# Performance work log

Measured on AMD Instinct MI355X. Metric: run time of the kernel, lower is better.

Reference implementation:

```python
import jax, jax.numpy as jnp
import numpy as np
from jax import lax


def _conv2d(x, w, b, stride):
    # x: [B,C,H,W], w: [O,I,kh,kw], b: [O]
    y = lax.conv_general_dilated(
        x, w, window_strides=(stride, stride), padding='VALID',
        dimension_numbers=('NCHW', 'OIHW', 'NCHW'))
    return y + b[None, :, None, None]


def setup_inputs() -> dict:
    key = jax.random.key(0)
    ks = jax.random.split(key, 4)
    B, C, H, W = 8, 128, 128, 128
    x = jax.random.normal(ks[0], (B, C, H, W), dtype=jnp.float32)
    # conv weights, scaled like torch default init (~1/sqrt(fan_in))
    Wq = jax.random.normal(ks[1], (C, C, 2, 2), dtype=jnp.float32) / np.sqrt(C * 4)
    Wk = jax.random.normal(ks[2], (C, C, 2, 2), dtype=jnp.float32) / np.sqrt(C * 4)
    Wv = jax.random.normal(ks[3], (C, C, 1, 1), dtype=jnp.float32) / np.sqrt(C)
    bq = jnp.zeros((C,), dtype=jnp.float32)
    bk = jnp.zeros((C,), dtype=jnp.float32)
    bv = jnp.zeros((C,), dtype=jnp.float32)
    return {'x': x, 'Wq': Wq, 'bq': bq, 'Wk': Wk, 'bk': bk, 'Wv': Wv, 'bv': bv}


def reference(x, Wq, bq, Wk, bk, Wv, bv):
    B, C, H, W = x.shape
    # query/key: 2x2 stride-2 convs -> [B, C, (H//2)*(W//2)]
    q = _conv2d(x, Wq, bq, 2).reshape(B, C, -1)
    k = _conv2d(x, Wk, bk, 2).reshape(B, C, -1)
    # value: 1x1 conv -> [B, C, H*W]
    v = _conv2d(x, Wv, bv, 1).reshape(B, C, -1)
    # energy: [B, C, C]
    energy = jnp.einsum('bcn,bdn->bcd', q, k)
    # max-subtract trick: softmax over (row_max - energy)
    energy_new = jnp.max(energy, axis=-1, keepdims=True) - energy
    attention = jax.nn.softmax(energy_new, axis=-1)
    out = jnp.einsum('bcd,bdn->bcn', attention, v)
    return out.reshape(B, C, H, W)
```

## Files before the change

### kernel.cpp

```cpp
#include <hip/hip_runtime.h>
#include <math.h>


typedef float f32x4 __attribute__((ext_vector_type(4)));
typedef short s16x8 __attribute__((ext_vector_type(8)));

__device__ __forceinline__ unsigned short f2bf(float f) {
  union { __bf16 b; unsigned short u; } v;
  v.b = (__bf16)f;
  return v.u;
}
__device__ __forceinline__ float bf2f(unsigned short h) {
  union { unsigned u; float f; } v; v.u = ((unsigned)h) << 16;
  return v.f;
}
__device__ __forceinline__ unsigned pack2(unsigned short a, unsigned short b) {
  return (unsigned)a | ((unsigned)b << 16);
}

__global__ __launch_bounds__(256) void k_prep(
    const float* __restrict__ Wq, const float* __restrict__ Wk,
    unsigned short* __restrict__ Wth, unsigned short* __restrict__ Wtl) {
  const int f = (blockIdx.x * 256 + threadIdx.x) * 4;
  const int row = f >> 9;
  const int k   = f & 511;
  const float* src = (row < 128) ? &Wq[row * 512 + k] : &Wk[(row - 128) * 512 + k];
  float4 v = *(const float4*)src;
  unsigned short h0 = f2bf(v.x), h1 = f2bf(v.y), h2 = f2bf(v.z), h3 = f2bf(v.w);
  unsigned short l0 = f2bf(v.x - bf2f(h0)), l1 = f2bf(v.y - bf2f(h1));
  unsigned short l2 = f2bf(v.z - bf2f(h2)), l3 = f2bf(v.w - bf2f(h3));
  const int di = (k >> 5) * 8192 + row * 32 + (k & 31);
  *(ushort4*)&Wth[di] = make_ushort4(h0, h1, h2, h3);
  *(ushort4*)&Wtl[di] = make_ushort4(l0, l1, l2, l3);
}

__global__ __launch_bounds__(256, 3) void k_conv_energy(
    const float* __restrict__ x,
    const unsigned short* __restrict__ Wth, const unsigned short* __restrict__ Wtl,
    const float* __restrict__ bq, const float* __restrict__ bk,
    float* __restrict__ epart) {
  __shared__ unsigned short LDS[16384];
  unsigned short* Th = LDS;
  unsigned short* Tl = LDS + 8192;

  const int t = threadIdx.x;
  const int nt = blockIdx.x, b = blockIdx.y;
  const int w = t >> 6, lane = t & 63;
  const int lrow = lane & 15, lkb = lane >> 4;

  const int pp = t >> 4;
  const int ci_l = pp >> 1, kh = pp & 1;
  const int i16 = t & 15;
  const int klb = ci_l * 4 + kh * 2;
  const float* xb = x + ((size_t)b << 21);
  const float* xrow = xb + (size_t)ci_l * 16384 + (2 * nt + kh) * 128 + 2 * i16;

  f32x4 acc[4][4];
#pragma unroll
  for (int m = 0; m < 4; ++m)
#pragma unroll
    for (int n = 0; n < 4; ++n) acc[m][n] = (f32x4){0.f, 0.f, 0.f, 0.f};

  s16x8 pfh[4], pfl[4];
  float2 pv[2][4];
  const int aoff = (w * 64 + lrow) * 32 + lkb * 8;

#pragma unroll
  for (int m = 0; m < 4; ++m) {
    pfh[m] = *(const s16x8*)&Wth[aoff + m * 512];
    pfl[m] = *(const s16x8*)&Wtl[aoff + m * 512];
  }
  {
    float2 v0 = *(const float2*)&xrow[0];
    float2 v1 = *(const float2*)&xrow[32];
    float2 v2 = *(const float2*)&xrow[64];
    float2 v3 = *(const float2*)&xrow[96];
    unsigned short hx, hy;
    hx = f2bf(v0.x); hy = f2bf(v0.y);
    *(unsigned*)&LDS[(i16     ) * 40 + klb] = pack2(hx, hy);
    *(unsigned*)&LDS[2560 + (i16     ) * 40 + klb] = pack2(f2bf(v0.x - bf2f(hx)), f2bf(v0.y - bf2f(hy)));
    hx = f2bf(v1.x); hy = f2bf(v1.y);
    *(unsigned*)&LDS[(i16 + 16) * 40 + klb] = pack2(hx, hy);
    *(unsigned*)&LDS[2560 + (i16 + 16) * 40 + klb] = pack2(f2bf(v1.x - bf2f(hx)), f2bf(v1.y - bf2f(hy)));
    hx = f2bf(v2.x); hy = f2bf(v2.y);
    *(unsigned*)&LDS[(i16 + 32) * 40 + klb] = pack2(hx, hy);
    *(unsigned*)&LDS[2560 + (i16 + 32) * 40 + klb] = pack2(f2bf(v2.x - bf2f(hx)), f2bf(v2.y - bf2f(hy)));
    hx = f2bf(v3.x); hy = f2bf(v3.y);
    *(unsigned*)&LDS[(i16 + 48) * 40 + klb] = pack2(hx, hy);
    *(unsigned*)&LDS[2560 + (i16 + 48) * 40 + klb] = pack2(f2bf(v3.x - bf2f(hx)), f2bf(v3.y - bf2f(hy)));
  }
#pragma unroll
  for (int g = 0; g < 4; ++g)
    pv[1][g] = *(const float2*)&xrow[(size_t)8 * 16384 + 32 * g];
  __syncthreads();

#pragma unroll
  for (int step = 0; step < 16; ++step) {
    const int cur = step & 1;
    const unsigned short* Bh = LDS + cur * 5120;
    const unsigned short* Bl = Bh + 2560;
    s16x8 bfh[4], bfl[4];
#pragma unroll
    for (int nf = 0; nf < 4; ++nf) {
      const int bidx = (nf * 16 + lrow) * 40 + lkb * 8;
      bfh[nf] = *(const s16x8*)&Bh[bidx];
      bfl[nf] = *(const s16x8*)&Bl[bidx];
    }
#pragma unroll
    for (int m = 0; m < 4; ++m)
#pragma unroll
      for (int n = 0; n < 4; ++n) {
        acc[m][n] = __builtin_amdgcn_mfma_f32_16x16x32_bf16(pfh[m], bfh[n], acc[m][n], 0, 0, 0);
        acc[m][n] = __builtin_amdgcn_mfma_f32_16x16x32_bf16(pfh[m], bfl[n], acc[m][n], 0, 0, 0);
        acc[m][n] = __builtin_amdgcn_mfma_f32_16x16x32_bf16(pfl[m], bfh[n], acc[m][n], 0, 0, 0);
      }
    if (step < 15) {
      const unsigned short* Wh_n = Wth + (step + 1) * 8192;
      const unsigned short* Wl_n = Wtl + (step + 1) * 8192;
#pragma unroll
      for (int m = 0; m < 4; ++m) {
        pfh[m] = *(const s16x8*)&Wh_n[aoff + m * 512];
        pfl[m] = *(const s16x8*)&Wl_n[aoff + m * 512];
      }
    }
    if (step < 14) {
#pragma unroll
      for (int g = 0; g < 4; ++g)
        pv[cur][g] = *(const float2*)&xrow[(size_t)(step + 2) * 8 * 16384 + 32 * g];
    }
    if (step < 15) {
      unsigned short* Nh = LDS + (cur ^ 1) * 5120;
      unsigned short* Nl = Nh + 2560;
#pragma unroll
      for (int g = 0; g < 4; ++g) {
        const int n = i16 + 16 * g;
        unsigned short hx = f2bf(pv[cur ^ 1][g].x), hy = f2bf(pv[cur ^ 1][g].y);
        *(unsigned*)&Nh[n * 40 + klb] = pack2(hx, hy);
        *(unsigned*)&Nl[n * 40 + klb] = pack2(f2bf(pv[cur ^ 1][g].x - bf2f(hx)),
                                              f2bf(pv[cur ^ 1][g].y - bf2f(hy)));
      }
      asm volatile("s_waitcnt lgkmcnt(0)" ::: "memory");
      __builtin_amdgcn_s_barrier();
    }
  }
  __syncthreads();

  const float* biasp = (w < 2) ? bq : bk;
  const int rb = (w & 1) * 64;
  float biasr[16];
#pragma unroll
  for (int m = 0; m < 4; ++m)
#pragma unroll
    for (int i = 0; i < 4; ++i)
      biasr[m * 4 + i] = biasp[rb + m * 16 + (lane >> 4) * 4 + i];

  f32x4 e[4][4];
#pragma unroll
  for (int m = 0; m < 4; ++m)
#pragma unroll
    for (int n = 0; n < 4; ++n) e[m][n] = (f32x4){0.f, 0.f, 0.f, 0.f};

  const int mrow0 = (w >> 1) * 64;
  const int nrow0 = 128 + (w & 1) * 64;

#pragma unroll
  for (int ks = 0; ks < 2; ++ks) {
#pragma unroll
    for (int m = 0; m < 4; ++m) {
      const int r0 = w * 64 + m * 16 + (lane >> 4) * 4;
#pragma unroll
      for (int nn = 0; nn < 2; ++nn) {
        const int n = 2 * ks + nn;
        const int cl = nn * 16 + lrow;
        const int cl8 = cl >> 3, c7 = cl & 7;
#pragma unroll
        for (int i = 0; i < 4; ++i) {
          const int r = r0 + i;
          const float vv = acc[m][n][i] + biasr[m * 4 + i];
          const unsigned short h = f2bf(vv);
          const unsigned short l = f2bf(vv - bf2f(h));
          const int ad = r * 32 + ((cl8 ^ (r & 3)) << 3) + c7;
          Th[ad] = h;
          Tl[ad] = l;
        }
      }
    }
    __syncthreads();
    {
      s16x8 qh[4], ql[4], kh8[4], kl8[4];
#pragma unroll
      for (int m = 0; m < 4; ++m) {
        const int r = mrow0 + m * 16 + lrow;
        const int ad = r * 32 + ((lkb ^ (r & 3)) << 3);
        qh[m] = *(const s16x8*)&Th[ad];
        ql[m] = *(const s16x8*)&Tl[ad];
      }
#pragma unroll
      for (int n = 0; n < 4; ++n) {
        const int r = nrow0 + n * 16 + lrow;
        const int ad = r * 32 + ((lkb ^ (r & 3)) << 3);
        kh8[n] = *(const s16x8*)&Th[ad];
        kl8[n] = *(const s16x8*)&Tl[ad];
      }
#pragma unroll
      for (int m = 0; m < 4; ++m)
#pragma unroll
        for (int n = 0; n < 4; ++n) {
          e[m][n] = __builtin_amdgcn_mfma_f32_16x16x32_bf16(qh[m], kh8[n], e[m][n], 0, 0, 0);
          e[m][n] = __builtin_amdgcn_mfma_f32_16x16x32_bf16(qh[m], kl8[n], e[m][n], 0, 0, 0);
          e[m][n] = __builtin_amdgcn_mfma_f32_16x16x32_bf16(ql[m], kh8[n], e[m][n], 0, 0, 0);
        }
    }
    if (ks == 0) __syncthreads();
  }

  float* ep = epart + ((size_t)b * 64 + nt) * 16384;
#pragma unroll
  for (int m = 0; m < 4; ++m) {
    const int qr = (w >> 1) * 64 + m * 16 + (lane >> 4) * 4;
#pragma unroll
    for (int n = 0; n < 4; ++n) {
      const int kr = (w & 1) * 64 + n * 16 + lrow;
#pragma unroll
      for (int i = 0; i < 4; ++i) ep[(size_t)(qr + i) * 128 + kr] = e[m][n][i];
    }
  }
}

__global__ __launch_bounds__(256) void k_softmax_M(
    const float* __restrict__ epart, const float* __restrict__ Wv,
    const float* __restrict__ bv, unsigned short* __restrict__ Mt,
    float* __restrict__ outbb) {
  __shared__ float As[4][128];
  const int t = threadIdx.x;
  const int wid = t >> 6, lane = t & 63;
  const int b = blockIdx.x >> 5;
  const int c = (blockIdx.x & 31) * 4 + wid;
  const int d0 = lane * 2;

  float2 s = make_float2(0.f, 0.f);
#pragma unroll 4
  for (int p = 0; p < 64; ++p) {
    float2 e = *(const float2*)&epart[((size_t)b * 64 + p) * 16384 + c * 128 + d0];
    s.x += e.x; s.y += e.y;
  }
  float mn = fminf(s.x, s.y);
#pragma unroll
  for (int off = 1; off < 64; off <<= 1) mn = fminf(mn, __shfl_xor(mn, off));
  const float p0 = expf(mn - s.x);
  const float p1 = expf(mn - s.y);
  float tot = p0 + p1;
#pragma unroll
  for (int off = 1; off < 64; off <<= 1) tot += __shfl_xor(tot, off);
  const float inv = 1.f / tot;
  const float a0 = p0 * inv, a1 = p1 * inv;

  const float2 bvv = *(const float2*)&bv[d0];
  float ob = a0 * bvv.x + a1 * bvv.y;
#pragma unroll
  for (int off = 1; off < 64; off <<= 1) ob += __shfl_xor(ob, off);
  if (lane == 0) outbb[b * 128 + c] = ob;

  As[wid][d0] = a0;
  As[wid][d0 + 1] = a1;
  float m0 = 0.f, m1 = 0.f;
#pragma unroll 4
  for (int d = 0; d < 128; ++d) {
    const float a = As[wid][d];
    const float2 wv = *(const float2*)&Wv[d * 128 + d0];
    m0 = fmaf(a, wv.x, m0);
    m1 = fmaf(a, wv.y, m1);
  }
  const int sk = lane >> 4;
  const int ko = (lane * 2) & 31;
  *(unsigned*)&Mt[(size_t)b * 16384 + sk * 4096 + c * 32 + ko] =
      pack2(f2bf(m0), f2bf(m1));
}

__global__ __launch_bounds__(256) void k_out(
    const float* __restrict__ x, const unsigned short* __restrict__ Mt,
    const float* __restrict__ outbb, float* __restrict__ out) {
  __shared__ unsigned short Xs[10240];
  const int t = threadIdx.x;
  const int nt = blockIdx.x, b = blockIdx.y;
  const int wid = t >> 6, lane = t & 63;
  const int wr = wid >> 1, wc = wid & 1;
  const int lrow = lane & 15, lkb = lane >> 4;
  const int xkl = (t >> 5) * 4;
  const int xc0 = (t & 31) * 4;

  const float* xb = x + ((size_t)b << 21);
  const unsigned short* Mb = Mt + (size_t)b * 16384;
  float* ob = out + ((size_t)b << 21);

  f32x4 acc[4][4];
#pragma unroll
  for (int m = 0; m < 4; ++m)
#pragma unroll
    for (int n = 0; n < 4; ++n) acc[m][n] = (f32x4){0.f, 0.f, 0.f, 0.f};

  float4 pv[2][4];
#pragma unroll
  for (int q = 0; q < 4; ++q) {
    float4 v = *(const float4*)&xb[(size_t)(xkl + q) * 16384 + nt * 128 + xc0];
    Xs[(xc0 + 0) * 40 + xkl + q] = f2bf(v.x);
    Xs[(xc0 + 1) * 40 + xkl + q] = f2bf(v.y);
    Xs[(xc0 + 2) * 40 + xkl + q] = f2bf(v.z);
    Xs[(xc0 + 3) * 40 + xkl + q] = f2bf(v.w);
  }
#pragma unroll
  for (int q = 0; q < 4; ++q)
    pv[1][q] = *(const float4*)&xb[(size_t)(32 + xkl + q) * 16384 + nt * 128 + xc0];
  __syncthreads();

#pragma unroll
  for (int step = 0; step < 4; ++step) {
    const int cur = step & 1;
    const unsigned short* Bx = Xs + cur * 5120;
    s16x8 bf[4];
#pragma unroll
    for (int n = 0; n < 4; ++n)
      bf[n] = *(const s16x8*)&Bx[(wc * 64 + n * 16 + lrow) * 40 + lkb * 8];
    s16x8 af[4];
#pragma unroll
    for (int m = 0; m < 4; ++m)
      af[m] = *(const s16x8*)&Mb[step * 4096 + (wr * 64 + m * 16 + lrow) * 32 + lkb * 8];
    if (step < 2) {
#pragma unroll
      for (int q = 0; q < 4; ++q)
        pv[cur][q] = *(const float4*)&xb[(size_t)((step + 2) * 32 + xkl + q) * 16384 + nt * 128 + xc0];
    }
#pragma unroll
    for (int m = 0; m < 4; ++m)
#pragma unroll
      for (int n = 0; n < 4; ++n)
        acc[m][n] = __builtin_amdgcn_mfma_f32_16x16x32_bf16(af[m], bf[n], acc[m][n], 0, 0, 0);
    if (step < 3) {
      unsigned short* Nx = Xs + (cur ^ 1) * 5120;
#pragma unroll
      for (int q = 0; q < 4; ++q) {
        Nx[(xc0 + 0) * 40 + xkl + q] = f2bf(pv[cur ^ 1][q].x);
        Nx[(xc0 + 1) * 40 + xkl + q] = f2bf(pv[cur ^ 1][q].y);
        Nx[(xc0 + 2) * 40 + xkl + q] = f2bf(pv[cur ^ 1][q].z);
        Nx[(xc0 + 3) * 40 + xkl + q] = f2bf(pv[cur ^ 1][q].w);
      }
      asm volatile("s_waitcnt lgkmcnt(0)" ::: "memory");
      __builtin_amdgcn_s_barrier();
    }
  }
#pragma unroll
  for (int m = 0; m < 4; ++m) {
    const int r0 = wr * 64 + m * 16 + (lane >> 4) * 4;
#pragma unroll
    for (int n = 0; n < 4; ++n) {
      const int gc = nt * 128 + wc * 64 + n * 16 + (lane & 15);
#pragma unroll
      for (int i = 0; i < 4; ++i) {
        const int row = r0 + i;
        ob[(size_t)row * 16384 + gc] = acc[m][n][i] + outbb[b * 128 + row];
      }
    }
  }
}

extern "C" void kernel_launch(void* const* d_in, const int* in_sizes, int n_in,
                              void* d_out, int out_size, void* d_ws, size_t ws_size,
                              hipStream_t stream) {
  const float* x  = (const float*)d_in[0];
  const float* Wq = (const float*)d_in[1];
  const float* bq = (const float*)d_in[2];
  const float* Wk = (const float*)d_in[3];
  const float* bk = (const float*)d_in[4];
  const float* Wv = (const float*)d_in[5];
  const float* bv = (const float*)d_in[6];
  float* out = (float*)d_out;
  char* ws = (char*)d_ws;

  float* epart = (float*)ws;
  unsigned short* Mt = (unsigned short*)(ws + 33554432);
  float* outbb = (float*)(ws + 33816576);
  unsigned short* Wth = (unsigned short*)(ws + 33820672);
  unsigned short* Wtl = (unsigned short*)(ws + 34082816);

  hipLaunchKernelGGL(k_prep, dim3(128), dim3(256), 0, stream, Wq, Wk, Wth, Wtl);
  hipLaunchKernelGGL(k_conv_energy, dim3(64, 8), dim3(256), 0, stream,
                     x, Wth, Wtl, bq, bk, epart);
  hipLaunchKernelGGL(k_softmax_M, dim3(256), dim3(256), 0, stream,
                     epart, Wv, bv, Mt, outbb);
  hipLaunchKernelGGL(k_out, dim3(128, 8), dim3(256), 0, stream,
                     x, Mt, outbb, out);
}
```

Baseline: 81.10 us.

## Use four LDS stages to halve barriers in conv-energy K loop

Grows the LDS staging for the x tile from two to four buffers, fills two stages up front, and prefetches global x loads three steps ahead instead of two. The block barrier now runs only every other step, which cuts synchronisation cost in the 16-step MFMA loop. In exchange the kernel uses more shared memory (40KB), which may limit the three-blocks-per-CU occupancy target and adds register pressure.

```diff
diff --git a/kernel.cpp b/kernel.cpp
--- a/kernel.cpp
+++ b/kernel.cpp
@@ -39,7 +39,7 @@
     const unsigned short* __restrict__ Wth, const unsigned short* __restrict__ Wtl,
     const float* __restrict__ bq, const float* __restrict__ bk,
     float* __restrict__ epart) {
-  __shared__ unsigned short LDS[16384];
+  __shared__ unsigned short LDS[20480];
   unsigned short* Th = LDS;
   unsigned short* Tl = LDS + 8192;
 
@@ -70,34 +70,28 @@
     pfh[m] = *(const s16x8*)&Wth[aoff + m * 512];
     pfl[m] = *(const s16x8*)&Wtl[aoff + m * 512];
   }
-  {
-    float2 v0 = *(const float2*)&xrow[0];
-    float2 v1 = *(const float2*)&xrow[32];
-    float2 v2 = *(const float2*)&xrow[64];
-    float2 v3 = *(const float2*)&xrow[96];
-    unsigned short hx, hy;
-    hx = f2bf(v0.x); hy = f2bf(v0.y);
-    *(unsigned*)&LDS[(i16     ) * 40 + klb] = pack2(hx, hy);
-    *(unsigned*)&LDS[2560 + (i16     ) * 40 + klb] = pack2(f2bf(v0.x - bf2f(hx)), f2bf(v0.y - bf2f(hy)));
-    hx = f2bf(v1.x); hy = f2bf(v1.y);
-    *(unsigned*)&LDS[(i16 + 16) * 40 + klb] = pack2(hx, hy);
-    *(unsigned*)&LDS[2560 + (i16 + 16) * 40 + klb] = pack2(f2bf(v1.x - bf2f(hx)), f2bf(v1.y - bf2f(hy)));
-    hx = f2bf(v2.x); hy = f2bf(v2.y);
-    *(unsigned*)&LDS[(i16 + 32) * 40 + klb] = pack2(hx, hy);
-    *(unsigned*)&LDS[2560 + (i16 + 32) * 40 + klb] = pack2(f2bf(v2.x - bf2f(hx)), f2bf(v2.y - bf2f(hy)));
-    hx = f2bf(v3.x); hy = f2bf(v3.y);
-    *(unsigned*)&LDS[(i16 + 48) * 40 + klb] = pack2(hx, hy);
-    *(unsigned*)&LDS[2560 + (i16 + 48) * 40 + klb] = pack2(f2bf(v3.x - bf2f(hx)), f2bf(v3.y - bf2f(hy)));
+#pragma unroll
+  for (int s0 = 0; s0 < 2; ++s0) {
+    unsigned short* Nh = LDS + s0 * 5120;
+    unsigned short* Nl = Nh + 2560;
+    const float* xr = xrow + (size_t)s0 * 8 * 16384;
+#pragma unroll
+    for (int g = 0; g < 4; ++g) {
+      float2 v = *(const float2*)&xr[32 * g];
+      const int n = i16 + 16 * g;
+      unsigned short hx = f2bf(v.x), hy = f2bf(v.y);
+      *(unsigned*)&Nh[n * 40 + klb] = pack2(hx, hy);
+      *(unsigned*)&Nl[n * 40 + klb] = pack2(f2bf(v.x - bf2f(hx)), f2bf(v.y - bf2f(hy)));
+    }
   }
 #pragma unroll
   for (int g = 0; g < 4; ++g)
-    pv[1][g] = *(const float2*)&xrow[(size_t)8 * 16384 + 32 * g];
+    pv[0][g] = *(const float2*)&xrow[(size_t)2 * 8 * 16384 + 32 * g];
   __syncthreads();
 
 #pragma unroll
   for (int step = 0; step < 16; ++step) {
-    const int cur = step & 1;
-    const unsigned short* Bh = LDS + cur * 5120;
+    const unsigned short* Bh = LDS + (step & 3) * 5120;
     const unsigned short* Bl = Bh + 2560;
     s16x8 bfh[4], bfl[4];
 #pragma unroll
@@ -123,22 +117,25 @@
         pfl[m] = *(const s16x8*)&Wl_n[aoff + m * 512];
       }
     }
-    if (step < 14) {
+    if (step + 3 < 16) {
 #pragma unroll
       for (int g = 0; g < 4; ++g)
-        pv[cur][g] = *(const float2*)&xrow[(size_t)(step + 2) * 8 * 16384 + 32 * g];
-    }
-    if (step < 15) {
-      unsigned short* Nh = LDS + (cur ^ 1) * 5120;
+        pv[(step + 1) & 1][g] =
+            *(const float2*)&xrow[(size_t)(step + 3) * 8 * 16384 + 32 * g];
+    }
+    if (step + 2 < 16) {
+      unsigned short* Nh = LDS + ((step + 2) & 3) * 5120;
       unsigned short* Nl = Nh + 2560;
 #pragma unroll
       for (int g = 0; g < 4; ++g) {
         const int n = i16 + 16 * g;
-        unsigned short hx = f2bf(pv[cur ^ 1][g].x), hy = f2bf(pv[cur ^ 1][g].y);
+        unsigned short hx = f2bf(pv[step & 1][g].x), hy = f2bf(pv[step & 1][g].y);
         *(unsigned*)&Nh[n * 40 + klb] = pack2(hx, hy);
-        *(unsigned*)&Nl[n * 40 + klb] = pack2(f2bf(pv[cur ^ 1][g].x - bf2f(hx)),
-                                              f2bf(pv[cur ^ 1][g].y - bf2f(hy)));
-      }
+        *(unsigned*)&Nl[n * 40 + klb] = pack2(f2bf(pv[step & 1][g].x - bf2f(hx)),
+                                              f2bf(pv[step & 1][g].y - bf2f(hy)));
+      }
+    }
+    if ((step & 1) == 1 && step < 15) {
       asm volatile("s_waitcnt lgkmcnt(0)" ::: "memory");
       __builtin_amdgcn_s_barrier();
     }
```

After: 82.86 us. 2.2% more time.
